# Performance work log

Hardware: AMD Instinct MI355X
Metric: run time of the kernel (lower is better)

Reference implementation:

```python
import jax, jax.numpy as jnp
import numpy as np

K = 4096          # num_embeddings
D = 256           # embedding_dim
BETA = 0.25
DECAY = 0.99
EPS = 1e-05

def setup_inputs() -> dict:
    key = jax.random.key(0)
    k1, k2, k3 = jax.random.split(key, 3)
    N = 65536
    return {
        "z": jax.random.normal(k1, (N, D), dtype=jnp.float32),
        "weight": jax.random.normal(k2, (K, D), dtype=jnp.float32),
        "ema_w": jax.random.normal(k3, (K, D), dtype=jnp.float32),
        "ema_cluster_size": jnp.ones((K,), dtype=jnp.float32),
    }

def reference(z, weight, ema_w, ema_cluster_size):
    # pairwise squared distances: [N, K]
    d = (jnp.sum(z * z, axis=1, keepdims=True)
         + jnp.sum(weight * weight, axis=1)
         - 2.0 * jnp.matmul(z, weight.T))
    idx = jnp.argmin(d, axis=1)                     # [N]
    encodings = jax.nn.one_hot(idx, K, dtype=z.dtype)  # [N, K]

    # EMA codebook update (training branch). In torch the results are re-wrapped
    # into fresh nn.Parameters, which detaches them from the autograd graph.
    def _ema(z_, enc_, ema_w_, cs_):
        cs = cs_ * DECAY + (1.0 - DECAY) * jnp.sum(enc_, axis=0)
        n = jnp.sum(cs)
        cs = (cs + EPS) / (n + K * EPS) * n
        dw = jnp.matmul(enc_.T, z_)                 # [K, D] scatter-add of z by code
        new_ema_w = ema_w_ * DECAY + (1.0 - DECAY) * dw
        new_weight = new_ema_w / cs[:, None]
        return cs, new_ema_w, new_weight
    new_cs, new_ema_w, new_weight = jax.lax.stop_gradient(
        _ema(z, encodings, ema_w, ema_cluster_size))

    z_q = new_weight[idx]                           # [N, D] gather from updated codebook
    loss = (jnp.mean((jax.lax.stop_gradient(z_q) - z) ** 2)
            + BETA * jnp.mean((z_q - jax.lax.stop_gradient(z)) ** 2))
    avg_probs = jnp.mean(encodings, axis=0)
    perplexity = jnp.exp(-jnp.sum(avg_probs * jnp.log(avg_probs + 1e-10)))
    z_q = z + jax.lax.stop_gradient(z_q - z)        # straight-through estimator
    return (z_q, idx[:, None], loss, perplexity, new_cs, new_ema_w, new_weight)
```

## Files before the change

kernel.cpp:

```cpp
#include <hip/hip_runtime.h>
#include <math.h>

#define NPTS 65536
#define DIMD 256
#define KCB  4096
#define MARGIN 2.0f

#define O_ZQ   0
#define O_IDX  16777216
#define O_LOSS 16842752
#define O_PERP 16842753
#define O_CS   16842754
#define O_EMAW 16846850
#define O_W    17895426

#define OFF_WSW   8388608
#define OFF_CCNT  8912896
#define OFF_CIDS  8978432
#define OFF_OFFS  10027008
#define OFF_CUR   10031232
#define OFF_ROWS  10035328
#define OFF_GMIN  10100864
#define OFF_CHOF  10166400
#define OFF_BMIN  10240000
#define OFF_RL    11288576

#define CHK 64
#define MAXCHUNKS 5120
#define PADL 65600

#define RING0 4
#define NSLOT 64

typedef __attribute__((ext_vector_type(8))) short short8;
typedef __attribute__((ext_vector_type(4))) float f32x4;

__device__ __forceinline__ unsigned short f2bf(float f) {
    unsigned u = __float_as_uint(f);
    return (unsigned short)((u + 0x7FFF + ((u >> 16) & 1)) >> 16);
}
__device__ __forceinline__ unsigned encf(float f) {
    unsigned u = __float_as_uint(f);
    return (u >> 31) ? ~u : (u | 0x80000000u);
}
__device__ __forceinline__ float decf(unsigned e) {
    unsigned u = (e & 0x80000000u) ? (e & 0x7fffffffu) : ~e;
    return __uint_as_float(u);
}

__global__ void k_prep(const float* __restrict__ zsrc, const float* __restrict__ wsrc,
                       unsigned* __restrict__ zdst, unsigned* __restrict__ wdst,
                       float* __restrict__ zz, float* __restrict__ wwg,
                       unsigned* __restrict__ gmin, int* __restrict__ ccnt,
                       float* __restrict__ cs, float* __restrict__ scal,
                       int* __restrict__ bcnt) {
    int b = blockIdx.x, t = threadIdx.x;
    int l = t & 63;
    if (b < NPTS / 4) {
        int row = b * 4 + (t >> 6);
        float4 v = ((const float4*)(zsrc + (size_t)row * DIMD))[l];
        uint2 pk = make_uint2(f2bf(v.x) | (f2bf(v.y) << 16),
                              f2bf(v.z) | (f2bf(v.w) << 16));
        ((uint2*)zdst)[(size_t)row * 64 + l] = pk;
        float s = v.x*v.x + v.y*v.y + v.z*v.z + v.w*v.w;
        #pragma unroll
        for (int off = 32; off; off >>= 1) s += __shfl_down(s, off);
        if (l == 0) zz[row] = s;
        if (t < 4) gmin[b * 4 + t] = 0xFFFFFFFFu;
        else if (t < 8) ccnt[b * 4 + (t - 4)] = 0;
    } else {
        int b2 = b - NPTS / 4;
        int row = b2 * 4 + (t >> 6);
        float4 v = ((const float4*)(wsrc + (size_t)row * DIMD))[l];
        uint2 pk = make_uint2(f2bf(v.x) | (f2bf(v.y) << 16),
                              f2bf(v.z) | (f2bf(v.w) << 16));
        int g = row >> 4, n16 = row & 15;
        int c = l >> 3, q = (l >> 1) & 3, half = l & 1;
        ((uint2*)wdst)[g * 1024 + c * 128 + (q * 16 + n16) * 2 + half] = pk;
        float s = v.x*v.x + v.y*v.y + v.z*v.z + v.w*v.w;
        #pragma unroll
        for (int off = 32; off; off >>= 1) s += __shfl_down(s, off);
        if (l == 0) wwg[row] = s;
        if (t < 4) cs[b2 * 4 + t] = 0.f;
        if (b2 == 0) { scal[t] = 0.f; if (t < 16) bcnt[t] = 0; }
    }
}

__launch_bounds__(256, 2)
__global__ void k_pass0(const unsigned* __restrict__ zbf,
                        const uint4* __restrict__ wsw4,
                        const float* __restrict__ wwg,
                        unsigned* __restrict__ gmin,
                        float* __restrict__ bmin) {
    __shared__ __align__(16) char smem[RING0 * 16384];
    __shared__ float lds_ww[2048];
    const int t = threadIdx.x, wv = t >> 6, l = t & 63;
    const int q = l >> 4, n16 = l & 15;
    const int rb    = blockIdx.x >> 1;
    const int half  = blockIdx.x & 1;
    const int row0  = rb * 256 + wv * 64;
    const int g0    = half * 128;
    const int ph0s  = ((blockIdx.x * 3) & 7) * 8;

    union U { uint4 u; short8 s; } afr[4][8];
    #pragma unroll
    for (int s = 0; s < 4; ++s) {
        const char* zb = (const char*)zbf + ((size_t)(row0 + s * 16 + n16) << 9) + q * 16;
        #pragma unroll
        for (int c = 0; c < 8; ++c) afr[s][c].u = *(const uint4*)(zb + c * 64);
    }

    auto stage = [&](int buf, int s) {
        const int sa = (ph0s + s) & 63;
        const uint4* srcb = wsw4 + (size_t)(g0 + sa * 2) * 512;
        #pragma unroll
        for (int j = 0; j < 4; ++j) {
            int rrow = j * 4 + wv;
            __builtin_amdgcn_global_load_lds(
                (const __attribute__((address_space(1))) unsigned*)(srcb + rrow * 64 + l),
                (__attribute__((address_space(3))) unsigned*)(&smem[buf * 16384 + rrow * 1024]),
                16, 0, 0);
        }
    };

    for (int i = t; i < 2048; i += 256) lds_ww[i] = wwg[g0 * 16 + i];
    stage(0, 0);
    stage(1, 1);
    __syncthreads();

    float minv[16], bm[16];
    #pragma unroll
    for (int i = 0; i < 16; ++i) { minv[i] = 3.0e38f; bm[i] = 3.0e38f; }

    int buf = 0, sbuf = 2;
    #pragma unroll 1
    for (int s = 0; s < NSLOT; ++s) {
        if (s < NSLOT - 2) {
            stage(sbuf, s + 2);
            sbuf = (sbuf + 1) & 3;
            asm volatile("s_waitcnt vmcnt(8)" ::: "memory");
        } else {
            asm volatile("s_waitcnt vmcnt(0)" ::: "memory");
        }
        __builtin_amdgcn_s_barrier();
        const char* sbase = smem + buf * 16384;
        buf = (buf + 1) & 3;
        const int sa = (ph0s + s) & 63;
        #pragma unroll
        for (int g2 = 0; g2 < 2; ++g2) {
            f32x4 acc[4];
            #pragma unroll
            for (int s4 = 0; s4 < 4; ++s4) acc[s4] = (f32x4){0.f, 0.f, 0.f, 0.f};
            __builtin_amdgcn_s_setprio(1);
            #pragma unroll
            for (int c = 0; c < 8; ++c) {
                U bf; bf.u = *(const uint4*)(sbase + g2 * 8192 + c * 1024 + (l << 4));
                #pragma unroll
                for (int s4 = 0; s4 < 4; ++s4)
                    acc[s4] = __builtin_amdgcn_mfma_f32_16x16x32_bf16(afr[s4][c].s, bf.s, acc[s4], 0, 0, 0);
            }
            __builtin_amdgcn_s_setprio(0);
            float wwv = lds_ww[(sa * 2 + g2) * 16 + n16];
            #pragma unroll
            for (int s4 = 0; s4 < 4; ++s4)
                #pragma unroll
                for (int r = 0; r < 4; ++r)
                    bm[s4*4+r] = fminf(bm[s4*4+r], fmaf(-2.f, acc[s4][r], wwv));
        }
        if ((s & 7) == 7) {
            const int blk = (g0 >> 4) + (((ph0s + (s & ~7)) & 63) >> 3);
            #pragma unroll
            for (int i = 0; i < 16; ++i) {
                float m = bm[i];
                minv[i] = fminf(minv[i], m);
                #pragma unroll
                for (int msk = 1; msk < 16; msk <<= 1) m = fminf(m, __shfl_xor(m, msk));
                if (n16 == 0)
                    bmin[(size_t)(row0 + (i >> 2) * 16 + q * 4 + (i & 3)) * 16 + blk] = m;
                bm[i] = 3.0e38f;
            }
        }
    }

    #pragma unroll
    for (int i = 0; i < 16; ++i) {
        float m = minv[i];
        #pragma unroll
        for (int msk = 1; msk < 16; msk <<= 1) m = fminf(m, __shfl_xor(m, msk));
        if (n16 == 0)
            atomicMin(&gmin[row0 + (i >> 2) * 16 + q * 4 + (i & 3)], encf(m));
    }
}

__global__ void k_bsel(const unsigned* __restrict__ gmin,
                       const float* __restrict__ bmin,
                       int* __restrict__ bcnt, int* __restrict__ rlist) {
    __shared__ int lcnt[16], lbase[16], lcur[16];
    int t = threadIdx.x;
    if (t < 16) { lcnt[t] = 0; lcur[t] = 0; }
    __syncthreads();
    int row = blockIdx.x * 256 + t;
    float thr = decf(gmin[row]) + MARGIN;
    const float* bm = bmin + (size_t)row * 16;
    unsigned qual = 0;
    #pragma unroll
    for (int b = 0; b < 16; ++b)
        if (bm[b] <= thr) { qual |= (1u << b); atomicAdd(&lcnt[b], 1); }
    __syncthreads();
    if (t < 16) lbase[t] = atomicAdd(&bcnt[t], lcnt[t]);
    __syncthreads();
    #pragma unroll
    for (int b = 0; b < 16; ++b)
        if (qual & (1u << b)) {
            int p = atomicAdd(&lcur[b], 1);
            rlist[b * PADL + lbase[b] + p] = row;
        }
}

__launch_bounds__(256, 2)
__global__ void k_pass1(const unsigned* __restrict__ zbf,
                        const uint4* __restrict__ wsw4,
                        const float* __restrict__ wwg,
                        const unsigned* __restrict__ gmin,
                        const int* __restrict__ bcnt,
                        const int* __restrict__ rlist,
                        int* __restrict__ ccnt,
                        int* __restrict__ cids) {
    const int t = threadIdx.x, wv = t >> 6, l = t & 63;
    const int q = l >> 4, n16 = l & 15;
    int bc[16];
    #pragma unroll
    for (int i = 0; i < 16; ++i) bc[i] = bcnt[i];
    int tp[17]; tp[0] = 0;
    #pragma unroll
    for (int i = 0; i < 16; ++i) tp[i + 1] = tp[i] + ((bc[i] + 63) >> 6);
    const int ntiles = tp[16];

    for (int tile = blockIdx.x * 4 + wv; tile < ntiles; tile += 2048) {
        int b = 0, tpb = 0, nb = bc[0];
        #pragma unroll
        for (int i = 1; i < 16; ++i)
            if (tp[i] <= tile) { b = i; tpb = tp[i]; nb = bc[i]; }
        const int lim = nb - (tile - tpb) * 64;
        const int* rl = rlist + b * PADL + (tile - tpb) * 64;

        union U { uint4 u; short8 s; } afr[4][8];
        #pragma unroll
        for (int s = 0; s < 4; ++s) {
            int idx = s * 16 + n16;
            int r = (idx < lim) ? rl[idx] : -1;
            int rr = r < 0 ? 0 : r;
            const char* zb = (const char*)zbf + ((size_t)rr << 9) + q * 16;
            #pragma unroll
            for (int c = 0; c < 8; ++c) afr[s][c].u = *(const uint4*)(zb + c * 64);
        }
        int rowid[16];
        float thr[16];
        #pragma unroll
        for (int i = 0; i < 16; ++i) {
            int idx = (i >> 2) * 16 + q * 4 + (i & 3);
            int r = (idx < lim) ? rl[idx] : -1;
            rowid[i] = r;
            thr[i] = -3.0e38f;
            if (r >= 0) thr[i] = decf(gmin[r]) + MARGIN;
        }

        #pragma unroll 2
        for (int g = 0; g < 16; ++g) {
            const int gg = b * 16 + g;
            const uint4* wp = wsw4 + (size_t)gg * 512 + l;
            f32x4 acc[4];
            #pragma unroll
            for (int s = 0; s < 4; ++s) acc[s] = (f32x4){0.f, 0.f, 0.f, 0.f};
            #pragma unroll
            for (int c = 0; c < 8; ++c) {
                U bf; bf.u = wp[c * 64];
                #pragma unroll
                for (int s = 0; s < 4; ++s)
                    acc[s] = __builtin_amdgcn_mfma_f32_16x16x32_bf16(afr[s][c].s, bf.s, acc[s], 0, 0, 0);
            }
            float wwv = wwg[gg * 16 + n16];
            #pragma unroll
            for (int s = 0; s < 4; ++s)
                #pragma unroll
                for (int r = 0; r < 4; ++r) {
                    float core = fmaf(-2.f, acc[s][r], wwv);
                    if (core <= thr[s*4+r]) {
                        int row = rowid[s * 4 + r];
                        int pos = atomicAdd(&ccnt[row], 1);
                        if (pos < 16) cids[row * 16 + pos] = gg * 16 + n16;
                    }
                }
        }
    }
}

__global__ void k_refine(const float* __restrict__ z,
                         const float* __restrict__ w,
                         const float* __restrict__ zz,
                         const float* __restrict__ wwg,
                         const int* __restrict__ ccnt,
                         const int* __restrict__ cids,
                         float* __restrict__ counts,
                         int*   __restrict__ idxi,
                         float* __restrict__ idxf) {
    int l   = threadIdx.x & 63;
    int row = blockIdx.x * 4 + (threadIdx.x >> 6);
    int n = ccnt[row]; if (n > 16) n = 16;
    float4 zv = ((const float4*)(z + (size_t)row * DIMD))[l];
    float zzv = zz[row];
    float bd = 3.0e38f; int bi = 0x7fffffff;
    for (int j = 0; j < n; ++j) {
        int k = cids[row * 16 + j];
        float4 wv = ((const float4*)(w + (size_t)k * DIMD))[l];
        float s = zv.x*wv.x + zv.y*wv.y + zv.z*wv.z + zv.w*wv.w;
        #pragma unroll
        for (int off = 32; off; off >>= 1) s += __shfl_xor(s, off);
        float d = (zzv + wwg[k]) - 2.0f * s;
        if (d < bd || (d == bd && k < bi)) { bd = d; bi = k; }
    }
    if (l == 0) {
        idxi[row] = bi;
        idxf[row] = (float)bi;
        atomicAdd(&counts[bi], 1.0f);
    }
}

__global__ void k_mid(const float* __restrict__ counts,
                      const float* __restrict__ ema_cs,
                      int* __restrict__ offs, int* __restrict__ cursor,
                      int* __restrict__ choffs,
                      float* __restrict__ cs_io, float* __restrict__ perp) {
    __shared__ int sc[1024];
    __shared__ float2 redf[16];
    int t = threadIdx.x;
    int c[4]; int s = 0;
    #pragma unroll
    for (int i = 0; i < 4; ++i) { c[i] = (int)counts[t * 4 + i]; s += c[i]; }
    sc[t] = s;
    __syncthreads();
    for (int d = 1; d < 1024; d <<= 1) {
        int v = (t >= d) ? sc[t - d] : 0;
        __syncthreads();
        sc[t] += v;
        __syncthreads();
    }
    int o = sc[t] - s;
    #pragma unroll
    for (int i = 0; i < 4; ++i) { offs[t*4+i] = o; cursor[t*4+i] = o; o += c[i]; }
    if (t == 1023) offs[4096] = sc[1023];
    __syncthreads();

    int ch[4]; int s2 = 0;
    #pragma unroll
    for (int i = 0; i < 4; ++i) { ch[i] = (c[i] + CHK - 1) / CHK; s2 += ch[i]; }
    sc[t] = s2;
    __syncthreads();
    for (int d = 1; d < 1024; d <<= 1) {
        int v = (t >= d) ? sc[t - d] : 0;
        __syncthreads();
        sc[t] += v;
        __syncthreads();
    }
    int o2 = sc[t] - s2;
    #pragma unroll
    for (int i = 0; i < 4; ++i) { choffs[t*4+i] = o2; o2 += ch[i]; }
    if (t == 1023) choffs[4096] = sc[1023];
    __syncthreads();

    float csd[4]; float nl = 0.f, el = 0.f;
    #pragma unroll
    for (int i = 0; i < 4; ++i) {
        float cf = (float)c[i];
        float cd = ema_cs[t * 4 + i] * 0.99f + 0.01f * cf;
        csd[i] = cd;
        nl += cd;
        float p = cf * (1.0f / 65536.0f);
        el += p * logf(p + 1e-10f);
    }
    #pragma unroll
    for (int off = 32; off; off >>= 1) { nl += __shfl_down(nl, off); el += __shfl_down(el, off); }
    if ((t & 63) == 0) redf[t >> 6] = make_float2(nl, el);
    __syncthreads();
    if (t == 0) {
        float n = 0.f, e = 0.f;
        for (int i = 0; i < 16; ++i) { n += redf[i].x; e += redf[i].y; }
        redf[0] = make_float2(n, e);
        perp[0] = expf(-e);
    }
    __syncthreads();
    float n = redf[0].x;
    float scale = n / (n + 4096.0f * 1e-5f);
    #pragma unroll
    for (int i = 0; i < 4; ++i)
        cs_io[t * 4 + i] = (csd[i] + 1e-5f) * scale;
}

__global__ void k_fill(const int* __restrict__ idxi, int* __restrict__ cursor,
                       int* __restrict__ rows, float* __restrict__ dw) {
    int r = blockIdx.x * 256 + threadIdx.x;
    float4* p = (float4*)(dw + (size_t)r * 16);
    float4 zf = make_float4(0.f, 0.f, 0.f, 0.f);
    p[0] = zf; p[1] = zf; p[2] = zf; p[3] = zf;
    int k = idxi[r];
    int pos = atomicAdd(&cursor[k], 1);
    rows[pos] = r;
}

__global__ void k_dw(const float* __restrict__ z, const int* __restrict__ offs,
                     const int* __restrict__ choffs, const int* __restrict__ rows,
                     float* __restrict__ dw) {
    __shared__ float4 part[4][64];
    int b = blockIdx.x;
    if (b >= choffs[KCB]) return;
    int lo = 0, hi = KCB;
    while (hi - lo > 1) { int mid = (lo + hi) >> 1; if (choffs[mid] <= b) lo = mid; else hi = mid; }
    int k  = lo;
    int ci = b - choffs[k];
    int o0 = offs[k] + ci * CHK;
    int o1 = offs[k + 1]; if (o1 > o0 + CHK) o1 = o0 + CHK;
    int l = threadIdx.x & 63, j = threadIdx.x >> 6;
    float4 a = make_float4(0.f, 0.f, 0.f, 0.f);
    for (int i = o0 + j; i < o1; i += 4) {
        int r = rows[i];
        float4 v = ((const float4*)(z + (size_t)r * DIMD))[l];
        a.x += v.x; a.y += v.y; a.z += v.z; a.w += v.w;
    }
    part[j][l] = a;
    __syncthreads();
    if (j == 0) {
        float4 bb = part[0][l], c = part[1][l], d = part[2][l], e = part[3][l];
        a = make_float4(bb.x+c.x+d.x+e.x, bb.y+c.y+d.y+e.y,
                        bb.z+c.z+d.z+e.z, bb.w+c.w+d.w+e.w);
        float* p = dw + (size_t)k * DIMD + l * 4;
        if (choffs[k + 1] - choffs[k] == 1) {
            *(float4*)p = a;
        } else {
            atomicAdd(p + 0, a.x); atomicAdd(p + 1, a.y);
            atomicAdd(p + 2, a.z); atomicAdd(p + 3, a.w);
        }
    }
}

__global__ void k_emaw(const float* __restrict__ ema_w,
                       const float* __restrict__ cs,
                       float* __restrict__ emaw_io,
                       float* __restrict__ wout) {
    int i = (blockIdx.x * 256 + threadIdx.x) * 4;
    int k = i >> 8;
    float4 dv = *(const float4*)(emaw_io + i);
    float4 ev = *(const float4*)(ema_w + i);
    float c = cs[k];
    float4 ne;
    ne.x = ev.x * 0.99f + 0.01f * dv.x;
    ne.y = ev.y * 0.99f + 0.01f * dv.y;
    ne.z = ev.z * 0.99f + 0.01f * dv.z;
    ne.w = ev.w * 0.99f + 0.01f * dv.w;
    *(float4*)(emaw_io + i) = ne;
    float4 nw = make_float4(ne.x / c, ne.y / c, ne.z / c, ne.w / c);
    *(float4*)(wout + i) = nw;
}

__global__ void k_zq(const float* __restrict__ z,
                     const float* __restrict__ wnew,
                     const int* __restrict__ idxi,
                     float* __restrict__ zq,
                     float* __restrict__ sqacc) {
    __shared__ float red[4];
    int i = (blockIdx.x * 256 + threadIdx.x) * 4;
    int n = i >> 8;
    int d = i & 255;
    int k = idxi[n];
    float4 wv = *(const float4*)(wnew + (k << 8) + d);
    float4 zv = *(const float4*)(z + i);
    float4 o;
    o.x = zv.x + (wv.x - zv.x);
    o.y = zv.y + (wv.y - zv.y);
    o.z = zv.z + (wv.z - zv.z);
    o.w = zv.w + (wv.w - zv.w);
    *(float4*)(zq + i) = o;
    float dx = wv.x - zv.x, dy = wv.y - zv.y, dz = wv.z - zv.z, dw_ = wv.w - zv.w;
    float s = dx*dx + dy*dy + dz*dz + dw_*dw_;
    #pragma unroll
    for (int off = 32; off; off >>= 1) s += __shfl_down(s, off);
    int lane = threadIdx.x & 63;
    if (lane == 0) red[threadIdx.x >> 6] = s;
    __syncthreads();
    if (threadIdx.x == 0)
        atomicAdd(&sqacc[blockIdx.x & 255], red[0] + red[1] + red[2] + red[3]);
}

__global__ void k_final(const float* __restrict__ sqacc, float* __restrict__ loss) {
    __shared__ float red[4];
    int t = threadIdx.x;
    float s = sqacc[t];
    #pragma unroll
    for (int off = 32; off; off >>= 1) s += __shfl_down(s, off);
    if ((t & 63) == 0) red[t >> 6] = s;
    __syncthreads();
    if (t == 0)
        loss[0] = 1.25f * (red[0] + red[1] + red[2] + red[3]) * (1.0f / 16777216.0f);
}

extern "C" void kernel_launch(void* const* d_in, const int* in_sizes, int n_in,
                              void* d_out, int out_size, void* d_ws, size_t ws_size,
                              hipStream_t stream) {
    const float* z      = (const float*)d_in[0];
    const float* weight = (const float*)d_in[1];
    const float* ema_w  = (const float*)d_in[2];
    const float* ema_cs = (const float*)d_in[3];
    float* out = (float*)d_out;
    float* ws  = (float*)d_ws;

    int*   bcnt = (int*)ws;
    float* scal = ws + 4096;
    int*   idxi = (int*)(ws + 8192);

    unsigned* zbf    = (unsigned*)(out + O_ZQ);
    uint4*    wsw4   = (uint4*)(out + O_ZQ + OFF_WSW);
    int*      ccnt   = (int*)(out + O_ZQ + OFF_CCNT);
    int*      cids   = (int*)(out + O_ZQ + OFF_CIDS);
    int*      offs   = (int*)(out + O_ZQ + OFF_OFFS);
    int*      cursor = (int*)(out + O_ZQ + OFF_CUR);
    int*      rows   = (int*)(out + O_ZQ + OFF_ROWS);
    unsigned* gmin   = (unsigned*)(out + O_ZQ + OFF_GMIN);
    int*      choffs = (int*)(out + O_ZQ + OFF_CHOF);
    float*    bmin   = out + O_ZQ + OFF_BMIN;
    int*      rlist  = (int*)(out + O_ZQ + OFF_RL);
    float*    zz     = out + O_EMAW;
    float*    wwg    = out + O_EMAW + 65536;

    k_prep   <<<NPTS / 4 + KCB / 4, 256, 0, stream>>>(z, weight, zbf,
                                                      (unsigned*)wsw4, zz, wwg,
                                                      gmin, ccnt, out + O_CS,
                                                      scal, bcnt);
    k_pass0  <<<512, 256, 0, stream>>>(zbf, wsw4, wwg, gmin, bmin);
    k_bsel   <<<NPTS / 256, 256, 0, stream>>>(gmin, bmin, bcnt, rlist);
    k_pass1  <<<512, 256, 0, stream>>>(zbf, wsw4, wwg, gmin, bcnt, rlist,
                                       ccnt, cids);
    k_refine <<<NPTS / 4, 256, 0, stream>>>(z, weight, zz, wwg, ccnt, cids,
                                            out + O_CS, idxi, out + O_IDX);
    k_mid    <<<1, 1024, 0, stream>>>(out + O_CS, ema_cs, offs, cursor, choffs,
                                      out + O_CS, out + O_PERP);
    k_fill   <<<NPTS / 256, 256, 0, stream>>>(idxi, cursor, rows, out + O_EMAW);
    k_dw     <<<MAXCHUNKS, 256, 0, stream>>>(z, offs, choffs, rows, out + O_EMAW);
    k_emaw   <<<(KCB * DIMD) / 1024, 256, 0, stream>>>(ema_w, out + O_CS,
                                                       out + O_EMAW, out + O_W);
    k_zq     <<<(NPTS * DIMD) / 1024, 256, 0, stream>>>(z, out + O_W, idxi,
                                                        out + O_ZQ, scal);
    k_final  <<<1, 256, 0, stream>>>(scal, out + O_LOSS);
}
```

Baseline: 441.2 us.

## Fold codebook norm bias into MFMA init and fuse tail kernels via last-block tickets

In pass0 the MFMA accumulators are initialised with -0.5*||w||^2, and a max-reduction replaces the per-element fma plus min, with a -2 rescale applied only when storing. k_mid is merged into k_refine and k_final into k_zq: the last block to finish, found through an atomic ticket counter, does the scan, perplexity and loss reduction. This removes two tiny single-block launches and some VALU work in the hot loop. The cost is a serialized tail in the last block, with 256 threads handling 16 entries each, and reliance on threadfence and atomic ordering being correct.

```diff
diff --git a/kernel.cpp b/kernel.cpp
--- a/kernel.cpp
+++ b/kernel.cpp
@@ -53,7 +53,7 @@
                        float* __restrict__ zz, float* __restrict__ wwg,
                        unsigned* __restrict__ gmin, int* __restrict__ ccnt,
                        float* __restrict__ cs, float* __restrict__ scal,
-                       int* __restrict__ bcnt) {
+                       int* __restrict__ bcnt, unsigned* __restrict__ ticks) {
     int b = blockIdx.x, t = threadIdx.x;
     int l = t & 63;
     if (b < NPTS / 4) {
@@ -82,7 +82,11 @@
         for (int off = 32; off; off >>= 1) s += __shfl_down(s, off);
         if (l == 0) wwg[row] = s;
         if (t < 4) cs[b2 * 4 + t] = 0.f;
-        if (b2 == 0) { scal[t] = 0.f; if (t < 16) bcnt[t] = 0; }
+        if (b2 == 0) {
+            scal[t] = 0.f;
+            if (t < 16) bcnt[t] = 0;
+            if (t < 2)  ticks[t] = 0u;
+        }
     }
 }
 
@@ -130,7 +134,7 @@
 
     float minv[16], bm[16];
     #pragma unroll
-    for (int i = 0; i < 16; ++i) { minv[i] = 3.0e38f; bm[i] = 3.0e38f; }
+    for (int i = 0; i < 16; ++i) { minv[i] = -3.0e38f; bm[i] = -3.0e38f; }
 
     int buf = 0, sbuf = 2;
     #pragma unroll 1
@@ -148,9 +152,10 @@
         const int sa = (ph0s + s) & 63;
         #pragma unroll
         for (int g2 = 0; g2 < 2; ++g2) {
+            float bias = -0.5f * lds_ww[(sa * 2 + g2) * 16 + n16];
             f32x4 acc[4];
             #pragma unroll
-            for (int s4 = 0; s4 < 4; ++s4) acc[s4] = (f32x4){0.f, 0.f, 0.f, 0.f};
+            for (int s4 = 0; s4 < 4; ++s4) acc[s4] = (f32x4){bias, bias, bias, bias};
             __builtin_amdgcn_s_setprio(1);
             #pragma unroll
             for (int c = 0; c < 8; ++c) {
@@ -160,24 +165,23 @@
                     acc[s4] = __builtin_amdgcn_mfma_f32_16x16x32_bf16(afr[s4][c].s, bf.s, acc[s4], 0, 0, 0);
             }
             __builtin_amdgcn_s_setprio(0);
-            float wwv = lds_ww[(sa * 2 + g2) * 16 + n16];
             #pragma unroll
             for (int s4 = 0; s4 < 4; ++s4)
                 #pragma unroll
                 for (int r = 0; r < 4; ++r)
-                    bm[s4*4+r] = fminf(bm[s4*4+r], fmaf(-2.f, acc[s4][r], wwv));
+                    bm[s4*4+r] = fmaxf(bm[s4*4+r], acc[s4][r]);
         }
         if ((s & 7) == 7) {
             const int blk = (g0 >> 4) + (((ph0s + (s & ~7)) & 63) >> 3);
             #pragma unroll
             for (int i = 0; i < 16; ++i) {
                 float m = bm[i];
-                minv[i] = fminf(minv[i], m);
+                minv[i] = fmaxf(minv[i], m);
                 #pragma unroll
-                for (int msk = 1; msk < 16; msk <<= 1) m = fminf(m, __shfl_xor(m, msk));
+                for (int msk = 1; msk < 16; msk <<= 1) m = fmaxf(m, __shfl_xor(m, msk));
                 if (n16 == 0)
-                    bmin[(size_t)(row0 + (i >> 2) * 16 + q * 4 + (i & 3)) * 16 + blk] = m;
-                bm[i] = 3.0e38f;
+                    bmin[(size_t)(row0 + (i >> 2) * 16 + q * 4 + (i & 3)) * 16 + blk] = -2.0f * m;
+                bm[i] = -3.0e38f;
             }
         }
     }
@@ -186,9 +190,9 @@
     for (int i = 0; i < 16; ++i) {
         float m = minv[i];
         #pragma unroll
-        for (int msk = 1; msk < 16; msk <<= 1) m = fminf(m, __shfl_xor(m, msk));
+        for (int msk = 1; msk < 16; msk <<= 1) m = fmaxf(m, __shfl_xor(m, msk));
         if (n16 == 0)
-            atomicMin(&gmin[row0 + (i >> 2) * 16 + q * 4 + (i & 3)], encf(m));
+            atomicMin(&gmin[row0 + (i >> 2) * 16 + q * 4 + (i & 3)], encf(-2.0f * m));
     }
 }
 
@@ -301,9 +305,18 @@
                          const float* __restrict__ wwg,
                          const int* __restrict__ ccnt,
                          const int* __restrict__ cids,
+                         const float* __restrict__ ema_cs,
                          float* __restrict__ counts,
                          int*   __restrict__ idxi,
-                         float* __restrict__ idxf) {
+                         float* __restrict__ idxf,
+                         int* __restrict__ offs, int* __restrict__ cursor,
+                         int* __restrict__ choffs,
+                         float* __restrict__ perp,
+                         unsigned* __restrict__ tick) {
+    __shared__ int lastb;
+    __shared__ int sc[256];
+    __shared__ float2 redf[4];
+    __shared__ float sn;
     int l   = threadIdx.x & 63;
     int row = blockIdx.x * 4 + (threadIdx.x >> 6);
     int n = ccnt[row]; if (n > 16) n = 16;
@@ -324,22 +337,27 @@
         idxf[row] = (float)bi;
         atomicAdd(&counts[bi], 1.0f);
     }
-}
-
-__global__ void k_mid(const float* __restrict__ counts,
-                      const float* __restrict__ ema_cs,
-                      int* __restrict__ offs, int* __restrict__ cursor,
-                      int* __restrict__ choffs,
-                      float* __restrict__ cs_io, float* __restrict__ perp) {
-    __shared__ int sc[1024];
-    __shared__ float2 redf[16];
+
+    __syncthreads();
+    if (threadIdx.x == 0) {
+        __threadfence();
+        lastb = (atomicAdd(tick, 1u) == (unsigned)(gridDim.x - 1)) ? 1 : 0;
+    }
+    __syncthreads();
+    if (!lastb) return;
+    __threadfence();
+
     int t = threadIdx.x;
-    int c[4]; int s = 0;
-    #pragma unroll
-    for (int i = 0; i < 4; ++i) { c[i] = (int)counts[t * 4 + i]; s += c[i]; }
+    int c[16]; int s = 0;
+    #pragma unroll
+    for (int i = 0; i < 16; ++i) {
+        c[i] = (int)__hip_atomic_load(&counts[t * 16 + i], __ATOMIC_RELAXED,
+                                      __HIP_MEMORY_SCOPE_AGENT);
+        s += c[i];
+    }
     sc[t] = s;
     __syncthreads();
-    for (int d = 1; d < 1024; d <<= 1) {
+    for (int d = 1; d < 256; d <<= 1) {
         int v = (t >= d) ? sc[t - d] : 0;
         __syncthreads();
         sc[t] += v;
@@ -347,16 +365,16 @@
     }
     int o = sc[t] - s;
     #pragma unroll
-    for (int i = 0; i < 4; ++i) { offs[t*4+i] = o; cursor[t*4+i] = o; o += c[i]; }
-    if (t == 1023) offs[4096] = sc[1023];
-    __syncthreads();
-
-    int ch[4]; int s2 = 0;
-    #pragma unroll
-    for (int i = 0; i < 4; ++i) { ch[i] = (c[i] + CHK - 1) / CHK; s2 += ch[i]; }
+    for (int i = 0; i < 16; ++i) { offs[t*16+i] = o; cursor[t*16+i] = o; o += c[i]; }
+    if (t == 255) offs[4096] = sc[255];
+    __syncthreads();
+
+    int ch[16]; int s2 = 0;
+    #pragma unroll
+    for (int i = 0; i < 16; ++i) { ch[i] = (c[i] + CHK - 1) / CHK; s2 += ch[i]; }
     sc[t] = s2;
     __syncthreads();
-    for (int d = 1; d < 1024; d <<= 1) {
+    for (int d = 1; d < 256; d <<= 1) {
         int v = (t >= d) ? sc[t - d] : 0;
         __syncthreads();
         sc[t] += v;
@@ -364,15 +382,14 @@
     }
     int o2 = sc[t] - s2;
     #pragma unroll
-    for (int i = 0; i < 4; ++i) { choffs[t*4+i] = o2; o2 += ch[i]; }
-    if (t == 1023) choffs[4096] = sc[1023];
-    __syncthreads();
-
-    float csd[4]; float nl = 0.f, el = 0.f;
-    #pragma unroll
-    for (int i = 0; i < 4; ++i) {
+    for (int i = 0; i < 16; ++i) { choffs[t*16+i] = o2; o2 += ch[i]; }
+    if (t == 255) choffs[4096] = sc[255];
+
+    float csd[16]; float nl = 0.f, el = 0.f;
+    #pragma unroll
+    for (int i = 0; i < 16; ++i) {
         float cf = (float)c[i];
-        float cd = ema_cs[t * 4 + i] * 0.99f + 0.01f * cf;
+        float cd = ema_cs[t * 16 + i] * 0.99f + 0.01f * cf;
         csd[i] = cd;
         nl += cd;
         float p = cf * (1.0f / 65536.0f);
@@ -383,17 +400,17 @@
     if ((t & 63) == 0) redf[t >> 6] = make_float2(nl, el);
     __syncthreads();
     if (t == 0) {
-        float n = 0.f, e = 0.f;
-        for (int i = 0; i < 16; ++i) { n += redf[i].x; e += redf[i].y; }
-        redf[0] = make_float2(n, e);
+        float nn = 0.f, e = 0.f;
+        for (int i = 0; i < 4; ++i) { nn += redf[i].x; e += redf[i].y; }
+        sn = nn;
         perp[0] = expf(-e);
     }
     __syncthreads();
-    float n = redf[0].x;
-    float scale = n / (n + 4096.0f * 1e-5f);
-    #pragma unroll
-    for (int i = 0; i < 4; ++i)
-        cs_io[t * 4 + i] = (csd[i] + 1e-5f) * scale;
+    float nn = sn;
+    float scale = nn / (nn + 4096.0f * 1e-5f);
+    #pragma unroll
+    for (int i = 0; i < 16; ++i)
+        counts[t * 16 + i] = (csd[i] + 1e-5f) * scale;
 }
 
 __global__ void k_fill(const int* __restrict__ idxi, int* __restrict__ cursor,
@@ -465,8 +482,11 @@
                      const float* __restrict__ wnew,
                      const int* __restrict__ idxi,
                      float* __restrict__ zq,
-                     float* __restrict__ sqacc) {
+                     float* __restrict__ sqacc,
+                     unsigned* __restrict__ tick,
+                     float* __restrict__ loss) {
     __shared__ float red[4];
+    __shared__ int lastb;
     int i = (blockIdx.x * 256 + threadIdx.x) * 4;
     int n = i >> 8;
     int d = i & 255;
@@ -486,17 +506,19 @@
     int lane = threadIdx.x & 63;
     if (lane == 0) red[threadIdx.x >> 6] = s;
     __syncthreads();
-    if (threadIdx.x == 0)
+    if (threadIdx.x == 0) {
         atomicAdd(&sqacc[blockIdx.x & 255], red[0] + red[1] + red[2] + red[3]);
-}
-
-__global__ void k_final(const float* __restrict__ sqacc, float* __restrict__ loss) {
-    __shared__ float red[4];
+        __threadfence();
+        lastb = (atomicAdd(tick, 1u) == (unsigned)(gridDim.x - 1)) ? 1 : 0;
+    }
+    __syncthreads();
+    if (!lastb) return;
+    __threadfence();
     int t = threadIdx.x;
-    float s = sqacc[t];
-    #pragma unroll
-    for (int off = 32; off; off >>= 1) s += __shfl_down(s, off);
-    if ((t & 63) == 0) red[t >> 6] = s;
+    float s2 = __hip_atomic_load(&sqacc[t], __ATOMIC_RELAXED, __HIP_MEMORY_SCOPE_AGENT);
+    #pragma unroll
+    for (int off = 32; off; off >>= 1) s2 += __shfl_down(s2, off);
+    if ((t & 63) == 0) red[t >> 6] = s2;
     __syncthreads();
     if (t == 0)
         loss[0] = 1.25f * (red[0] + red[1] + red[2] + red[3]) * (1.0f / 16777216.0f);
@@ -512,9 +534,10 @@
     float* out = (float*)d_out;
     float* ws  = (float*)d_ws;
 
-    int*   bcnt = (int*)ws;
-    float* scal = ws + 4096;
-    int*   idxi = (int*)(ws + 8192);
+    int*      bcnt  = (int*)ws;
+    float*    scal  = ws + 4096;
+    unsigned* ticks = (unsigned*)(ws + 4608);
+    int*      idxi  = (int*)(ws + 8192);
 
     unsigned* zbf    = (unsigned*)(out + O_ZQ);
     uint4*    wsw4   = (uint4*)(out + O_ZQ + OFF_WSW);
@@ -533,20 +556,20 @@
     k_prep   <<<NPTS / 4 + KCB / 4, 256, 0, stream>>>(z, weight, zbf,
                                                       (unsigned*)wsw4, zz, wwg,
                                                       gmin, ccnt, out + O_CS,
-                                                      scal, bcnt);
+                                                      scal, bcnt, ticks);
     k_pass0  <<<512, 256, 0, stream>>>(zbf, wsw4, wwg, gmin, bmin);
     k_bsel   <<<NPTS / 256, 256, 0, stream>>>(gmin, bmin, bcnt, rlist);
     k_pass1  <<<512, 256, 0, stream>>>(zbf, wsw4, wwg, gmin, bcnt, rlist,
                                        ccnt, cids);
     k_refine <<<NPTS / 4, 256, 0, stream>>>(z, weight, zz, wwg, ccnt, cids,
-                                            out + O_CS, idxi, out + O_IDX);
-    k_mid    <<<1, 1024, 0, stream>>>(out + O_CS, ema_cs, offs, cursor, choffs,
-                                      out + O_CS, out + O_PERP);
+                                            ema_cs, out + O_CS, idxi,
+                                            out + O_IDX, offs, cursor, choffs,
+                                            out + O_PERP, ticks + 0);
     k_fill   <<<NPTS / 256, 256, 0, stream>>>(idxi, cursor, rows, out + O_EMAW);
     k_dw     <<<MAXCHUNKS, 256, 0, stream>>>(z, offs, choffs, rows, out + O_EMAW);
     k_emaw   <<<(KCB * DIMD) / 1024, 256, 0, stream>>>(ema_w, out + O_CS,
                                                        out + O_EMAW, out + O_W);
     k_zq     <<<(NPTS * DIMD) / 1024, 256, 0, stream>>>(z, out + O_W, idxi,
-                                                        out + O_ZQ, scal);
-    k_final  <<<1, 256, 0, stream>>>(scal, out + O_LOSS);
-}
+                                                        out + O_ZQ, scal,
+                                                        ticks + 1, out + O_LOSS);
+}
```

New measurement: 1.330 ms. +201.6%, slower.
